# Kernel tuning notes

Measured on AMD Instinct MI355X. Metric: run time of the kernel, lower is better.

Reference implementation:

```python
import jax, jax.numpy as jnp
import numpy as np

TAU = 2.0        # LIF membrane time constant
ALPHA = 4.0      # spikingjelly default Sigmoid surrogate alpha
NUM_HEADS = 8

@jax.custom_vjp
def spike(x):
    return (x >= 0.0).astype(x.dtype)

def _spike_fwd(x):
    return spike(x), x

def _spike_bwd(x, g):
    s = jax.nn.sigmoid(ALPHA * x)
    return (g * ALPHA * s * (1.0 - s),)

spike.defvjp(_spike_fwd, _spike_bwd)

def lif(x_seq, v_th):
    """Multi-step LIF over leading time dim. Hard reset to 0, detach_reset."""
    def step(v, xt):
        h = v + (xt - v) / TAU
        s = spike(h - v_th)
        v_new = h * (1.0 - jax.lax.stop_gradient(s))
        return v_new, s
    _, s_seq = jax.lax.scan(step, jnp.zeros_like(x_seq[0]), x_seq)
    return s_seq

def bn_eval(x, w, b, m, v, eps=1e-5):
    # BatchNorm1d in eval mode over channel dim C (last axis here, since the
    # torch code transposes to (TB,C,N) purely to make C the channel axis).
    inv = w / jnp.sqrt(v + eps)
    return x * inv + (b - m * inv)

def setup_inputs() -> dict:
    key = jax.random.key(0)
    T, B, N, C = 4, 8, 512, 512
    ks = jax.random.split(key, 32)
    d = {"x": jax.random.normal(ks[0], (T, B, N, C), dtype=jnp.float32)}
    names = ["q", "k", "v", "p"]
    for i, nm in enumerate(names):
        kk = jax.random.split(ks[i + 1], 6)
        d[nm + "_w"] = jax.random.normal(kk[0], (C, C), dtype=jnp.float32) * (C ** -0.5)
        d[nm + "_b"] = jax.random.normal(kk[1], (C,), dtype=jnp.float32) * 0.01
        d[nm + "_bn_w"] = jax.random.uniform(kk[2], (C,), minval=0.5, maxval=1.5, dtype=jnp.float32)
        d[nm + "_bn_b"] = jax.random.normal(kk[3], (C,), dtype=jnp.float32) * 0.1
        d[nm + "_bn_m"] = jax.random.normal(kk[4], (C,), dtype=jnp.float32) * 0.1
        d[nm + "_bn_v"] = jax.random.uniform(kk[5], (C,), minval=0.5, maxval=1.5, dtype=jnp.float32)
    return d

def _forward(x, q_w, q_b, q_bn_w, q_bn_b, q_bn_m, q_bn_v,
             k_w, k_b, k_bn_w, k_bn_b, k_bn_m, k_bn_v,
             v_w, v_b, v_bn_w, v_bn_b, v_bn_m, v_bn_v,
             p_w, p_b, p_bn_w, p_bn_b, p_bn_m, p_bn_v):
    T, B, N, C = x.shape
    H = NUM_HEADS
    hd = C // H
    scale = hd ** -0.5

    def branch(w, b, bw, bb, bm, bv):
        y = jnp.einsum("tbnc,dc->tbnd", x, w) + b            # Linear
        y = bn_eval(y, bw, bb, bm, bv)                        # BN1d (eval)
        y = lif(y, 1.0)                                       # (T,B,N,C) spikes
        return y.reshape(T, B, N, H, hd).transpose(0, 1, 3, 2, 4)  # (T,B,H,N,hd)

    q = branch(q_w, q_b, q_bn_w, q_bn_b, q_bn_m, q_bn_v)
    k = branch(k_w, k_b, k_bn_w, k_bn_b, k_bn_m, k_bn_v)
    v = branch(v_w, v_b, v_bn_w, v_bn_b, v_bn_m, v_bn_v)

    gamma = 1.0 - 2.0 ** (-5.0 - jnp.arange(H, dtype=jnp.float32))
    idx = jnp.arange(N)
    dist = jnp.abs(idx[:, None] - idx[None, :]).astype(jnp.float32)  # bidirectional
    D = gamma[:, None, None] ** dist                                  # (H,N,N)

    attn = jnp.einsum("tbhnd,tbhmd->tbhnm", q, k) * scale * D
    out = jnp.einsum("tbhnm,tbhmd->tbhnd", attn, v)
    out = out.transpose(0, 1, 3, 2, 4).reshape(T, B, N, C)
    out = lif(out, 0.5)                                      # retention_lif, v_th=0.5

    y = jnp.einsum("tbnc,dc->tbnd", out, p_w) + p_b
    y = bn_eval(y, p_bn_w, p_bn_b, p_bn_m, p_bn_v)
    return lif(y, 1.0)

def reference(x, q_w, q_b, q_bn_w, q_bn_b, q_bn_m, q_bn_v,
              k_w, k_b, k_bn_w, k_bn_b, k_bn_m, k_bn_v,
              v_w, v_b, v_bn_w, v_bn_b, v_bn_m, v_bn_v,
              p_w, p_b, p_bn_w, p_bn_b, p_bn_m, p_bn_v):
    return _forward(x, q_w, q_b, q_bn_w, q_bn_b, q_bn_m, q_bn_v,
                    k_w, k_b, k_bn_w, k_bn_b, k_bn_m, k_bn_v,
                    v_w, v_b, v_bn_w, v_bn_b, v_bn_m, v_bn_v,
                    p_w, p_b, p_bn_w, p_bn_b, p_bn_m, p_bn_v)
```

## Files before the change

kernel.cpp:

```cpp
#include <hip/hip_runtime.h>
#include <cstdint>

typedef unsigned long long u64;

#define TPB 256
#define MARGIN 5e-4
#define FCAP (1 << 20)

typedef __bf16 bf16x8 __attribute__((ext_vector_type(8)));
typedef __bf16 bf16x4 __attribute__((ext_vector_type(4)));
typedef float f32x4 __attribute__((ext_vector_type(4)));

__global__ void init_kernel(double* __restrict__ pw, int* __restrict__ ctr) {
    int h = threadIdx.x;
    if (h < 8) {
        double gamma = 1.0 - ldexp(1.0, -5 - h);
        double p = 1.0;
        for (int i = 0; i < 512; ++i) { pw[h * 512 + i] = p; p *= gamma; }
        ctr[h] = 0;
    }
}

__global__ void split_all(const float* __restrict__ x,
                          const float* __restrict__ w0, const float* __restrict__ w1,
                          const float* __restrict__ w2, const float* __restrict__ w3,
                          __bf16* __restrict__ Xh, __bf16* __restrict__ Xl,
                          __bf16* __restrict__ Wsp) {
    int blk = blockIdx.x;
    const float* src; __bf16 *hi, *lo; size_t off;
    if (blk < 8192) {
        src = x; hi = Xh; lo = Xl; off = (size_t)blk * 1024;
    } else {
        int wb = blk - 8192;
        int br = wb >> 8;
        const float* ws[4] = {w0, w1, w2, w3};
        src = ws[br];
        hi = Wsp + (size_t)br * 524288;
        lo = hi + 262144;
        off = (size_t)(wb & 255) * 1024;
    }
    size_t i = off + threadIdx.x * 4;
    float4 v = *(const float4*)(src + i);
    bf16x4 h4, l4;
    #pragma unroll
    for (int e = 0; e < 4; ++e) {
        float f = (&v.x)[e];
        __bf16 hh = (__bf16)f;
        h4[e] = hh;
        l4[e] = (__bf16)(f - (float)hh);
    }
    *(bf16x4*)(hi + i) = h4;
    *(bf16x4*)(lo + i) = l4;
}

__global__ __launch_bounds__(256) void gemm_bn_mfma2(
    const __bf16* __restrict__ Ahg, const __bf16* __restrict__ Alg,
    const __bf16* __restrict__ Whg, const __bf16* __restrict__ Wlg,
    const float* __restrict__ bias,
    const float* __restrict__ bnw, const float* __restrict__ bnb,
    const float* __restrict__ bnm, const float* __restrict__ bnv,
    float* __restrict__ out, int asplit)
{
    __shared__ __bf16 AhS[128][40];
    __shared__ __bf16 AlS[128][40];
    __shared__ __bf16 WhS[128][40];
    __shared__ __bf16 WlS[128][40];

    const int tid = threadIdx.x;
    const int m0 = blockIdx.x * 128;
    const int d0 = blockIdx.y * 128;
    const int wv = tid >> 6;
    const int wm = wv >> 1;
    const int wd = wv & 1;
    const int lane = tid & 63;
    const int fr = lane & 15;
    const int fg = lane >> 4;
// ... 1 lines not shown
    const int sseg = (tid & 1) * 16;

    f32x4 acc[4][4];
    #pragma unroll
    for (int i = 0; i < 4; ++i)
        #pragma unroll
        for (int j = 0; j < 4; ++j)
            acc[i][j] = (f32x4){0.f, 0.f, 0.f, 0.f};

    for (int k0 = 0; k0 < 512; k0 += 32) {
        __syncthreads();
        {
            const __bf16* pa = Ahg + (size_t)(m0 + srow) * 512 + k0 + sseg;
            *(bf16x8*)&AhS[srow][sseg]     = *(const bf16x8*)pa;
            *(bf16x8*)&AhS[srow][sseg + 8] = *(const bf16x8*)(pa + 8);
            if (asplit) {
                const __bf16* pl = Alg + (size_t)(m0 + srow) * 512 + k0 + sseg;
                *(bf16x8*)&AlS[srow][sseg]     = *(const bf16x8*)pl;
                *(bf16x8*)&AlS[srow][sseg + 8] = *(const bf16x8*)(pl + 8);
            }
            const __bf16* pwh = Whg + (size_t)(d0 + srow) * 512 + k0 + sseg;
            const __bf16* pwl = Wlg + (size_t)(d0 + srow) * 512 + k0 + sseg;
            *(bf16x8*)&WhS[srow][sseg]     = *(const bf16x8*)pwh;
            *(bf16x8*)&WhS[srow][sseg + 8] = *(const bf16x8*)(pwh + 8);
            *(bf16x8*)&WlS[srow][sseg]     = *(const bf16x8*)pwl;
            *(bf16x8*)&WlS[srow][sseg + 8] = *(const bf16x8*)(pwl + 8);
        }
        __syncthreads();

        bf16x8 ah[4], bh[4], bl[4];
        #pragma unroll
        for (int i = 0; i < 4; ++i)
            ah[i] = *(const bf16x8*)&AhS[wm * 64 + i * 16 + fr][fg * 8];
        #pragma unroll
        for (int j = 0; j < 4; ++j) {
            bh[j] = *(const bf16x8*)&WhS[wd * 64 + j * 16 + fr][fg * 8];
            bl[j] = *(const bf16x8*)&WlS[wd * 64 + j * 16 + fr][fg * 8];
        }
        #pragma unroll
        for (int i = 0; i < 4; ++i)
            #pragma unroll
            for (int j = 0; j < 4; ++j) {
                acc[i][j] = __builtin_amdgcn_mfma_f32_16x16x32_bf16(ah[i], bh[j], acc[i][j], 0, 0, 0);
                acc[i][j] = __builtin_amdgcn_mfma_f32_16x16x32_bf16(ah[i], bl[j], acc[i][j], 0, 0, 0);
            }
        if (asplit) {
            bf16x8 al[4];
            #pragma unroll
            for (int i = 0; i < 4; ++i)
                al[i] = *(const bf16x8*)&AlS[wm * 64 + i * 16 + fr][fg * 8];
            #pragma unroll
            for (int i = 0; i < 4; ++i)
                #pragma unroll
                for (int j = 0; j < 4; ++j)
                    acc[i][j] = __builtin_amdgcn_mfma_f32_16x16x32_bf16(al[i], bh[j], acc[i][j], 0, 0, 0);
        }
    }

    #pragma unroll
    for (int j = 0; j < 4; ++j) {
        int d = d0 + wd * 64 + j * 16 + fr;
        double inv = (double)bnw[d] / sqrt((double)bnv[d] + 1e-5);
        double sh  = (double)bnb[d] - (double)bnm[d] * inv;
        double bs  = (double)bias[d];
        #pragma unroll
        for (int i = 0; i < 4; ++i) {
            #pragma unroll
            for (int reg = 0; reg < 4; ++reg) {
                int m = m0 + wm * 64 + i * 16 + fg * 4 + reg;
                out[(size_t)m * 512 + d] = (float)(((double)acc[i][j][reg] + bs) * inv + sh);
            }
        }
    }
}

__global__ __launch_bounds__(256) void gemm_bn_mfma(
    const float* __restrict__ A, const float* __restrict__ W,
    const float* __restrict__ bias,
    const float* __restrict__ bnw, const float* __restrict__ bnb,
    const float* __restrict__ bnm, const float* __restrict__ bnv,
    float* __restrict__ out)
{
    __shared__ __bf16 Ah[128][36];
    __shared__ __bf16 Al[128][36];
    __shared__ __bf16 Wh[64][36];
    __shared__ __bf16 Wl[64][36];

    const int tid = threadIdx.x;
    const int m0 = blockIdx.x * 128;
    const int d0 = blockIdx.y * 64;
    const int wv = tid >> 6;
    const int wm = wv >> 1;
    const int wd = wv & 1;
    const int lane = tid & 63;
    const int fr = lane & 15;
    const int fg = lane >> 4;
    const int srow = tid >> 3;
    const int scol = (tid & 7) * 4;

    f32x4 acc[4][2];
    #pragma unroll
    for (int i = 0; i < 4; ++i)
        #pragma unroll
        for (int j = 0; j < 2; ++j)
            acc[i][j] = (f32x4){0.f, 0.f, 0.f, 0.f};

    for (int k0 = 0; k0 < 512; k0 += 32) {
        __syncthreads();
        #pragma unroll
        for (int rep = 0; rep < 4; ++rep) {
            int row = srow + 32 * rep;
            float4 va = *(const float4*)(A + (size_t)(m0 + row) * 512 + k0 + scol);
            #pragma unroll
            for (int e = 0; e < 4; ++e) {
                float f = (&va.x)[e];
                __bf16 h = (__bf16)f;
                Ah[row][scol + e] = h;
                Al[row][scol + e] = (__bf16)(f - (float)h);
            }
        }
        #pragma unroll
        for (int rep = 0; rep < 2; ++rep) {
            int row = srow + 32 * rep;
            float4 vw = *(const float4*)(W + (size_t)(d0 + row) * 512 + k0 + scol);
            #pragma unroll
            for (int e = 0; e < 4; ++e) {
                float f = (&vw.x)[e];
                __bf16 h = (__bf16)f;
                Wh[row][scol + e] = h;
                Wl[row][scol + e] = (__bf16)(f - (float)h);
            }
        }
        __syncthreads();

        union FU { bf16x8 v8; struct { __bf16 a[4], b[4]; } s; };
        bf16x8 ah[4], al[4], bh[2], bl[2];
        #pragma unroll
        for (int i = 0; i < 4; ++i) {
            int row = wm * 64 + i * 16 + fr;
            FU u1, u2;
            *(double*)&u1.s.a[0] = *(const double*)&Ah[row][fg * 8];
            *(double*)&u1.s.b[0] = *(const double*)&Ah[row][fg * 8 + 4];
            *(double*)&u2.s.a[0] = *(const double*)&Al[row][fg * 8];
            *(double*)&u2.s.b[0] = *(const double*)&Al[row][fg * 8 + 4];
            ah[i] = u1.v8; al[i] = u2.v8;
        }
        #pragma unroll
        for (int j = 0; j < 2; ++j) {
            int row = wd * 32 + j * 16 + fr;
            FU u1, u2;
            *(double*)&u1.s.a[0] = *(const double*)&Wh[row][fg * 8];
            *(double*)&u1.s.b[0] = *(const double*)&Wh[row][fg * 8 + 4];
            *(double*)&u2.s.a[0] = *(const double*)&Wl[row][fg * 8];
            *(double*)&u2.s.b[0] = *(const double*)&Wl[row][fg * 8 + 4];
            bh[j] = u1.v8; bl[j] = u2.v8;
        }
        #pragma unroll
        for (int i = 0; i < 4; ++i)
            #pragma unroll
            for (int j = 0; j < 2; ++j) {
                acc[i][j] = __builtin_amdgcn_mfma_f32_16x16x32_bf16(ah[i], bh[j], acc[i][j], 0, 0, 0);
                acc[i][j] = __builtin_amdgcn_mfma_f32_16x16x32_bf16(ah[i], bl[j], acc[i][j], 0, 0, 0);
                acc[i][j] = __builtin_amdgcn_mfma_f32_16x16x32_bf16(al[i], bh[j], acc[i][j], 0, 0, 0);
            }
    }

    #pragma unroll
    for (int j = 0; j < 2; ++j) {
        int d = d0 + wd * 32 + j * 16 + fr;
        double inv = (double)bnw[d] / sqrt((double)bnv[d] + 1e-5);
        double sh  = (double)bnb[d] - (double)bnm[d] * inv;
        double bs  = (double)bias[d];
        #pragma unroll
        for (int i = 0; i < 4; ++i) {
            #pragma unroll
            for (int reg = 0; reg < 4; ++reg) {
                int m = m0 + wm * 64 + i * 16 + fg * 4 + reg;
                out[(size_t)m * 512 + d] = (float)(((double)acc[i][j][reg] + bs) * inv + sh);
            }
        }
    }
}

__global__ void lif_mask_flag(const float* __restrict__ Y, u64* __restrict__ msk,
                              int* __restrict__ ctr, int* __restrict__ list, int slot) {
    int g = blockIdx.x * TPB + threadIdx.x;
    int c = g & 511, n = (g >> 9) & 511, b = g >> 18;
    int h = c >> 6;
    int lane = threadIdx.x & 63;
    double v = 0.0;
    bool flag = false;
    for (int t = 0; t < 4; ++t) {
        float y = Y[((size_t)((t * 8 + b) * 512 + n) << 9) + c];
        double hh = v + ((double)y - v) * 0.5;
        flag |= fabs(hh - 1.0) < MARGIN;
        bool s = hh >= 1.0;
        u64 mk = __ballot(s);
        if (lane == 0) msk[((t * 8 + b) * 8 + h) * 512 + n] = mk;
        v = s ? 0.0 : hh;
    }
    if (flag) {
        int idx = atomicAdd(ctr + slot, 1);
        if (idx < FCAP) list[idx] = g;
    }
}

__global__ void fix_mask(const float* __restrict__ x, const float* __restrict__ w,
                         const float* __restrict__ bias,
                         const float* __restrict__ bnw, const float* __restrict__ bnb,
                         const float* __restrict__ bnm, const float* __restrict__ bnv,
                         u64* __restrict__ msk, const int* __restrict__ ctr,
                         const int* __restrict__ list, int slot) {
    int cnt = ctr[slot]; if (cnt > FCAP) cnt = FCAP;
    int wv = (blockIdx.x * blockDim.x + threadIdx.x) >> 6;
    int nw = (gridDim.x * blockDim.x) >> 6;
    int lane = threadIdx.x & 63;
    for (int i = wv; i < cnt; i += nw) {
        int g = list[i];
// ... 152 lines not shown
            }
        }
    }

    #pragma unroll
    for (int j2 = 0; j2 < 4; ++j2) {
        int c = h * 64 + j2 * 16 + fr;
        #pragma unroll
        for (int reg = 0; reg < 4; ++reg) {
            int n = n0 + wn + fg * 4 + reg;
            O[((size_t)(tb * 512 + n) << 9) + c] = acc_o[j2][reg];
        }
    }
}

__global__ void lif_ret_bf(const float* __restrict__ Y, __bf16* __restrict__ Rb,
                           int* __restrict__ ctr, int* __restrict__ list) {
    int g = blockIdx.x * TPB + threadIdx.x;
    int c = g & 511, n = (g >> 9) & 511, b = g >> 18;
    double v = 0.0, eb = 0.0;
    bool flag = false;
    for (int t = 0; t < 4; ++t) {
        size_t idx = ((size_t)((t * 8 + b) * 512 + n) << 9) + c;
        double x = (double)Y[idx];
        double hh = v + (x - v) * 0.5;
        eb = 0.5 * eb + 0.5 * (fabs(x) * 1e-4);
        flag |= fabs(hh - 0.5) <= eb + 1e-9;
        bool s = hh >= 0.5;
        Rb[idx] = s ? (__bf16)1.0f : (__bf16)0.0f;
        v = s ? 0.0 : hh;
        if (s) eb = 0.0;
    }
    if (flag) {
        int i2 = atomicAdd(ctr + 4, 1);
        if (i2 < FCAP) list[i2] = g;
    }
}

__global__ void lif_ret_f(const float* __restrict__ Y, float* __restrict__ R,
                          int* __restrict__ ctr, int* __restrict__ list) {
    int g = blockIdx.x * TPB + threadIdx.x;
    int c = g & 511, n = (g >> 9) & 511, b = g >> 18;
    double v = 0.0, eb = 0.0;
    bool flag = false;
    for (int t = 0; t < 4; ++t) {
        size_t idx = ((size_t)((t * 8 + b) * 512 + n) << 9) + c;
        double x = (double)Y[idx];
        double hh = v + (x - v) * 0.5;
        eb = 0.5 * eb + 0.5 * (fabs(x) * 1e-4);
        flag |= fabs(hh - 0.5) <= eb + 1e-9;
        bool s = hh >= 0.5;
        R[idx] = s ? 1.0f : 0.0f;
        v = s ? 0.0 : hh;
        if (s) eb = 0.0;
    }
    if (flag) {
        int i2 = atomicAdd(ctr + 4, 1);
        if (i2 < FCAP) list[i2] = g;
    }
}

__global__ void repair_ret_bf(const u64* __restrict__ qm, const u64* __restrict__ km,
                              const u64* __restrict__ vm, const double* __restrict__ pw,
                              const int* __restrict__ ctr, const int* __restrict__ list,
                              __bf16* __restrict__ Rb) {
    int cnt = ctr[4]; if (cnt > FCAP) cnt = FCAP;
    int wv = (blockIdx.x * blockDim.x + threadIdx.x) >> 6;
    int nw = (gridDim.x * blockDim.x) >> 6;
    int lane = threadIdx.x & 63;
    for (int i = wv; i < cnt; i += nw) {
        int g = list[i];
        int c = g & 511, n = (g >> 9) & 511, b = g >> 18;
        int h = c >> 6, d = c & 63;
        double acc_t[4];
        for (int t = 0; t < 4; ++t) {
            int base = ((t * 8 + b) * 8 + h) * 512;
            u64 qw = qm[base + n];
            double p = 0.0;
            for (int j = 0; j < 8; ++j) {
                int m = j * 64 + lane;
// ... 1 lines not shown
                u64 vvm = vm[base + m];
                if ((vvm >> d) & 1ull) {
                    int dist = n - m; if (dist < 0) dist = -dist;
                    p += (double)__popcll(qw & kk) * pw[h * 512 + dist];
                }
            }
            acc_t[t] = p;
        }
        #pragma unroll
        for (int off = 32; off; off >>= 1) {
            #pragma unroll
            for (int t = 0; t < 4; ++t) acc_t[t] += __shfl_xor(acc_t[t], off, 64);
        }
        if (lane == 0) {
            double v = 0.0;
            for (int t = 0; t < 4; ++t) {
                double x = acc_t[t] * 0.125;
                double hh = v + (x - v) * 0.5;
                bool s = hh >= 0.5;
                Rb[((size_t)((t * 8 + b) * 512 + n) << 9) + c] = s ? (__bf16)1.0f : (__bf16)0.0f;
                v = s ? 0.0 : hh;
            }
        }
    }
}

__global__ void repair_ret_f(const u64* __restrict__ qm, const u64* __restrict__ km,
                             const u64* __restrict__ vm, const double* __restrict__ pw,
                             const int* __restrict__ ctr, const int* __restrict__ list,
                             float* __restrict__ r) {
    int cnt = ctr[4]; if (cnt > FCAP) cnt = FCAP;
    int wv = (blockIdx.x * blockDim.x + threadIdx.x) >> 6;
    int nw = (gridDim.x * blockDim.x) >> 6;
    int lane = threadIdx.x & 63;
    for (int i = wv; i < cnt; i += nw) {
        int g = list[i];
        int c = g & 511, n = (g >> 9) & 511, b = g >> 18;
        int h = c >> 6, d = c & 63;
// ... 19 lines not shown
            for (int t = 0; t < 4; ++t) acc_t[t] += __shfl_xor(acc_t[t], off, 64);
        }
        if (lane == 0) {
            double v = 0.0;
            for (int t = 0; t < 4; ++t) {
                double x = acc_t[t] * 0.125;
                double hh = v + (x - v) * 0.5;
                bool s = hh >= 0.5;
                r[((size_t)((t * 8 + b) * 512 + n) << 9) + c] = s ? 1.0f : 0.0f;
                v = s ? 0.0 : hh;
            }
        }
    }
}

__global__ void final_lif_flag(float* __restrict__ Y, int* __restrict__ ctr,
                               int* __restrict__ list) {
    int g = blockIdx.x * TPB + threadIdx.x;
    int c = g & 511, n = (g >> 9) & 511, b = g >> 18;
    double v = 0.0;
    bool flag = false;
    for (int t = 0; t < 4; ++t) {
        size_t idx = ((size_t)((t * 8 + b) * 512 + n) << 9) + c;
        float y = Y[idx];
        double hh = v + ((double)y - v) * 0.5;
        flag |= fabs(hh - 1.0) < MARGIN;
        bool s = hh >= 1.0;
        Y[idx] = s ? 1.0f : 0.0f;
        v = s ? 0.0 : hh;
    }
    if (flag) {
        int idx = atomicAdd(ctr + 3, 1);
        if (idx < FCAP) list[idx] = g;
    }
}

__global__ void final_flag(const float* __restrict__ Y, int* __restrict__ ctr,
                           int* __restrict__ list) {
    int g = blockIdx.x * TPB + threadIdx.x;
    int c = g & 511, n = (g >> 9) & 511, b = g >> 18;
    double v = 0.0;
    bool flag = false;
    for (int t = 0; t < 4; ++t) {
        float y = Y[((size_t)((t * 8 + b) * 512 + n) << 9) + c];
        double hh = v + ((double)y - v) * 0.5;
        flag |= fabs(hh - 1.0) < MARGIN;
        bool s = hh >= 1.0;
        v = s ? 0.0 : hh;
    }
    if (flag) {
        int idx = atomicAdd(ctr + 3, 1);
        if (idx < FCAP) list[idx] = g;
    }
}

__global__ void final_write(const float* __restrict__ Y, float* __restrict__ out) {
    int g = blockIdx.x * TPB + threadIdx.x;
    int c = g & 511, n = (g >> 9) & 511, b = g >> 18;
    double v = 0.0;
    for (int t = 0; t < 4; ++t) {
        size_t idx = ((size_t)((t * 8 + b) * 512 + n) << 9) + c;
        float y = Y[idx];
        double hh = v + ((double)y - v) * 0.5;
        bool s = hh >= 1.0;
        out[idx] = s ? 1.0f : 0.0f;
        v = s ? 0.0 : hh;
    }
}

__global__ void fix_final_bf(const __bf16* __restrict__ rr, const float* __restrict__ w,
                             const float* __restrict__ bias,
                             const float* __restrict__ bnw, const float* __restrict__ bnb,
                             const float* __restrict__ bnm, const float* __restrict__ bnv,
                             const int* __restrict__ ctr, int* __restrict__ list) {
    int cnt = ctr[3]; if (cnt > FCAP) cnt = FCAP;
    int wv = (blockIdx.x * blockDim.x + threadIdx.x) >> 6;
    int nw = (gridDim.x * blockDim.x) >> 6;
    int lane = threadIdx.x & 63;
    for (int i = wv; i < cnt; i += nw) {
        int g = list[i] & 0x00FFFFFF;
        int c = g & 511, n = (g >> 9) & 511, b = g >> 18;
        const float* wr = w + (size_t)c * 512;
        double dot[4];
        #pragma unroll
        for (int t = 0; t < 4; ++t) {
            const __bf16* xr = rr + ((size_t)((t * 8 + b) * 512 + n) << 9);
            double p = 0.0;
            #pragma unroll
            for (int j = 0; j < 8; ++j)
                p += (double)(float)xr[lane + 64 * j] * (double)wr[lane + 64 * j];
            dot[t] = p;
        }
        #pragma unroll
        for (int off = 32; off; off >>= 1) {
            #pragma unroll
            for (int t = 0; t < 4; ++t)
                dot[t] += __shfl_xor(dot[t], off, 64);
        }
        if (lane == 0) {
            double inv = (double)bnw[c] / sqrt((double)bnv[c] + 1e-5);
            double sh  = (double)bnb[c] - (double)bnm[c] * inv;
            double bs  = (double)bias[c];
            double v = 0.0;
            int sp = 0;
            for (int t = 0; t < 4; ++t) {
                double y = (dot[t] + bs) * inv + sh;
                double hh = v + (y - v) * 0.5;
                bool s = hh >= 1.0;
                sp |= (s ? 1 : 0) << t;
                v = s ? 0.0 : hh;
            }
            list[i] = g | (sp << 24);
        }
    }
}

__global__ void fix_final_f(const float* __restrict__ rr, const float* __restrict__ w,
                            const float* __restrict__ bias,
                            const float* __restrict__ bnw, const float* __restrict__ bnb,
                            const float* __restrict__ bnm, const float* __restrict__ bnv,
                            const int* __restrict__ ctr, int* __restrict__ list) {
    int cnt = ctr[3]; if (cnt > FCAP) cnt = FCAP;
    int wv = (blockIdx.x * blockDim.x + threadIdx.x) >> 6;
    int nw = (gridDim.x * blockDim.x) >> 6;
    int lane = threadIdx.x & 63;
    for (int i = wv; i < cnt; i += nw) {
        int g = list[i] & 0x00FFFFFF;
        int c = g & 511, n = (g >> 9) & 511, b = g >> 18;
// ... 20 lines not shown
            double bs  = (double)bias[c];
            double v = 0.0;
            int sp = 0;
            for (int t = 0; t < 4; ++t) {
                double y = (dot[t] + bs) * inv + sh;
                double hh = v + (y - v) * 0.5;
                bool s = hh >= 1.0;
                sp |= (s ? 1 : 0) << t;
                v = s ? 0.0 : hh;
            }
            list[i] = g | (sp << 24);
        }
    }
}

__global__ void fix_scatter(const int* __restrict__ ctr, const int* __restrict__ list,
                            float* __restrict__ out) {
    int cnt = ctr[3]; if (cnt > FCAP) cnt = FCAP;
    int i = blockIdx.x * blockDim.x + threadIdx.x;
    if (i >= cnt) return;
    int e = list[i];
    int g = e & 0x00FFFFFF, sp = (e >> 24) & 0xF;
    int c = g & 511, n = (g >> 9) & 511, b = g >> 18;
    for (int t = 0; t < 4; ++t)
        out[((size_t)((t * 8 + b) * 512 + n) << 9) + c] = ((sp >> t) & 1) ? 1.0f : 0.0f;
}

extern "C" void kernel_launch(void* const* d_in, const int* in_sizes, int n_in,
                              void* d_out, int out_size, void* d_ws, size_t ws_size,
                              hipStream_t stream) {
// ... 21 lines not shown
    __bf16* Xh = (__bf16*)p;  p += NX * 2;
    __bf16* Xl = (__bf16*)p;  p += NX * 2;
    __bf16* Wsp = (__bf16*)p; p += (size_t)4 * 2 * 262144 * 2;
    size_t need_fast = (size_t)(p - (char*)d_ws);
    int fast = ws_size >= need_fast;

    init_kernel<<<1, 64, 0, stream>>>(pw, ctr);

    dim3 g2(128, 4);
    dim3 gg(128, 8);

    if (fast) {
        split_all<<<8192 + 1024, 256, 0, stream>>>(x, w[0], w[1], w[2], w[3], Xh, Xl, Wsp);
        for (int br = 0; br < 3; ++br) {
            u64* msk = br == 0 ? qm : (br == 1 ? km : vm);
            gemm_bn_mfma2<<<g2, 256, 0, stream>>>(Xh, Xl,
                Wsp + (size_t)br * 524288, Wsp + (size_t)br * 524288 + 262144,
                bi[br], bnw[br], bnb[br], bnm[br], bnv[br], Y, 1);
            lif_mask_flag<<<8192, TPB, 0, stream>>>(Y, msk, ctr, list, br);
            fix_mask<<<128, 256, 0, stream>>>(x, w[br], bi[br], bnw[br], bnb[br],
                                              bnm[br], bnv[br], msk, ctr, list, br);
        }
        ret_fused2<<<2048, 256, 0, stream>>>(qm, km, vm, pw, Y);
        lif_ret_bf<<<8192, TPB, 0, stream>>>(Y, Xh, ctr, list);
        repair_ret_bf<<<256, 256, 0, stream>>>(qm, km, vm, pw, ctr, list, Xh);
        gemm_bn_mfma2<<<g2, 256, 0, stream>>>(Xh, Xh,
            Wsp + (size_t)3 * 524288, Wsp + (size_t)3 * 524288 + 262144,
            bi[3], bnw[3], bnb[3], bnm[3], bnv[3], (float*)d_out, 0);
        final_lif_flag<<<8192, TPB, 0, stream>>>((float*)d_out, ctr, list);
        fix_final_bf<<<128, 256, 0, stream>>>(Xh, w[3], bi[3], bnw[3], bnb[3],
                                              bnm[3], bnv[3], ctr, list);
        fix_scatter<<<4096, 256, 0, stream>>>(ctr, list, (float*)d_out);
    } else {
        for (int br = 0; br < 3; ++br) {
            u64* msk = br == 0 ? qm : (br == 1 ? km : vm);
            gemm_bn_mfma<<<gg, 256, 0, stream>>>(x, w[br], bi[br], bnw[br], bnb[br],
                                                 bnm[br], bnv[br], Y);
            lif_mask_flag<<<8192, TPB, 0, stream>>>(Y, msk, ctr, list, br);
            fix_mask<<<128, 256, 0, stream>>>(x, w[br], bi[br], bnw[br], bnb[br],
                                              bnm[br], bnv[br], msk, ctr, list, br);
        }
        float* r = (float*)d_out;
        ret_fused2<<<2048, 256, 0, stream>>>(qm, km, vm, pw, Y);
        lif_ret_f<<<8192, TPB, 0, stream>>>(Y, r, ctr, list);
        repair_ret_f<<<256, 256, 0, stream>>>(qm, km, vm, pw, ctr, list, r);
        gemm_bn_mfma<<<gg, 256, 0, stream>>>(r, w[3], bi[3], bnw[3], bnb[3],
                                             bnm[3], bnv[3], Y);
// ... 8 lines not shown
```

Baseline: 326.9 us.

## Fuse LIF spike masking into GEMM epilogues and permute token layout

The bf16-split X is stored permuted so each GEMM tile row block holds all four timesteps of a token. That lets the LIF recurrence run inside the GEMM epilogue, writing bitmasks directly and removing the fp32 Y round trip and the separate lif_mask_flag kernel. The final projection GEMM likewise applies LIF and writes spikes straight to the output, with a direct fix kernel replacing the flag, fix and scatter passes. The retention LIF writes into the permuted layout, and the epilogue now does heavier double-precision work and scattered stores.

```diff
diff --git a/kernel.cpp b/kernel.cpp
--- a/kernel.cpp
+++ b/kernel.cpp
@@ -27,39 +27,51 @@
                           __bf16* __restrict__ Xh, __bf16* __restrict__ Xl,
                           __bf16* __restrict__ Wsp) {
     int blk = blockIdx.x;
-    const float* src; __bf16 *hi, *lo; size_t off;
     if (blk < 8192) {
-        src = x; hi = Xh; lo = Xl; off = (size_t)blk * 1024;
+        size_t i = (size_t)blk * 1024 + threadIdx.x * 4;
+        int m = (int)(i >> 9), c = (int)(i & 511);
+        int mp = (m & 4095) * 4 + (m >> 12);
+        float4 v = *(const float4*)(x + i);
+        bf16x4 h4, l4;
+        #pragma unroll
+        for (int e = 0; e < 4; ++e) {
+            float f = (&v.x)[e];
+            __bf16 hh = (__bf16)f;
+            h4[e] = hh;
+            l4[e] = (__bf16)(f - (float)hh);
+        }
+        size_t dst = (size_t)mp * 512 + c;
+        *(bf16x4*)(Xh + dst) = h4;
+        *(bf16x4*)(Xl + dst) = l4;
     } else {
         int wb = blk - 8192;
         int br = wb >> 8;
         const float* ws[4] = {w0, w1, w2, w3};
-        src = ws[br];
-        hi = Wsp + (size_t)br * 524288;
-        lo = hi + 262144;
-        off = (size_t)(wb & 255) * 1024;
-    }
-    size_t i = off + threadIdx.x * 4;
-    float4 v = *(const float4*)(src + i);
-    bf16x4 h4, l4;
-    #pragma unroll
-    for (int e = 0; e < 4; ++e) {
-        float f = (&v.x)[e];
-        __bf16 hh = (__bf16)f;
-        h4[e] = hh;
-        l4[e] = (__bf16)(f - (float)hh);
-    }
-    *(bf16x4*)(hi + i) = h4;
-    *(bf16x4*)(lo + i) = l4;
-}
-
-__global__ __launch_bounds__(256) void gemm_bn_mfma2(
+        const float* src = ws[br];
+        __bf16* hi = Wsp + (size_t)br * 524288;
+        __bf16* lo = hi + 262144;
+        size_t i = (size_t)(wb & 255) * 1024 + threadIdx.x * 4;
+        float4 v = *(const float4*)(src + i);
+        bf16x4 h4, l4;
+        #pragma unroll
+        for (int e = 0; e < 4; ++e) {
+            float f = (&v.x)[e];
+            __bf16 hh = (__bf16)f;
+            h4[e] = hh;
+            l4[e] = (__bf16)(f - (float)hh);
+        }
+        *(bf16x4*)(hi + i) = h4;
+        *(bf16x4*)(lo + i) = l4;
+    }
+}
+
+__global__ __launch_bounds__(256) void gemm_lif_mask(
     const __bf16* __restrict__ Ahg, const __bf16* __restrict__ Alg,
     const __bf16* __restrict__ Whg, const __bf16* __restrict__ Wlg,
     const float* __restrict__ bias,
     const float* __restrict__ bnw, const float* __restrict__ bnb,
     const float* __restrict__ bnm, const float* __restrict__ bnv,
-    float* __restrict__ out, int asplit)
+    u64* __restrict__ msk, int* __restrict__ ctr, int* __restrict__ list, int slot)
 {
     __shared__ __bf16 AhS[128][40];
     __shared__ __bf16 AlS[128][40];
@@ -91,11 +103,9 @@
             const __bf16* pa = Ahg + (size_t)(m0 + srow) * 512 + k0 + sseg;
             *(bf16x8*)&AhS[srow][sseg]     = *(const bf16x8*)pa;
             *(bf16x8*)&AhS[srow][sseg + 8] = *(const bf16x8*)(pa + 8);
-            if (asplit) {
-                const __bf16* pl = Alg + (size_t)(m0 + srow) * 512 + k0 + sseg;
-                *(bf16x8*)&AlS[srow][sseg]     = *(const bf16x8*)pl;
-                *(bf16x8*)&AlS[srow][sseg + 8] = *(const bf16x8*)(pl + 8);
-            }
+            const __bf16* pl = Alg + (size_t)(m0 + srow) * 512 + k0 + sseg;
+            *(bf16x8*)&AlS[srow][sseg]     = *(const bf16x8*)pl;
+            *(bf16x8*)&AlS[srow][sseg + 8] = *(const bf16x8*)(pl + 8);
             const __bf16* pwh = Whg + (size_t)(d0 + srow) * 512 + k0 + sseg;
             const __bf16* pwl = Wlg + (size_t)(d0 + srow) * 512 + k0 + sseg;
             *(bf16x8*)&WhS[srow][sseg]     = *(const bf16x8*)pwh;
@@ -121,164 +131,158 @@
                 acc[i][j] = __builtin_amdgcn_mfma_f32_16x16x32_bf16(ah[i], bh[j], acc[i][j], 0, 0, 0);
                 acc[i][j] = __builtin_amdgcn_mfma_f32_16x16x32_bf16(ah[i], bl[j], acc[i][j], 0, 0, 0);
             }
-        if (asplit) {
-            bf16x8 al[4];
-            #pragma unroll
-            for (int i = 0; i < 4; ++i)
-                al[i] = *(const bf16x8*)&AlS[wm * 64 + i * 16 + fr][fg * 8];
-            #pragma unroll
-            for (int i = 0; i < 4; ++i)
-                #pragma unroll
-                for (int j = 0; j < 4; ++j)
-                    acc[i][j] = __builtin_amdgcn_mfma_f32_16x16x32_bf16(al[i], bh[j], acc[i][j], 0, 0, 0);
-        }
-    }
-
+        bf16x8 al[4];
+        #pragma unroll
+        for (int i = 0; i < 4; ++i)
+            al[i] = *(const bf16x8*)&AlS[wm * 64 + i * 16 + fr][fg * 8];
+        #pragma unroll
+        for (int i = 0; i < 4; ++i)
+            #pragma unroll
+            for (int j = 0; j < 4; ++j)
+                acc[i][j] = __builtin_amdgcn_mfma_f32_16x16x32_bf16(al[i], bh[j], acc[i][j], 0, 0, 0);
+    }
+
+    double invj[4], shj[4], bsj[4];
     #pragma unroll
     for (int j = 0; j < 4; ++j) {
         int d = d0 + wd * 64 + j * 16 + fr;
-        double inv = (double)bnw[d] / sqrt((double)bnv[d] + 1e-5);
-        double sh  = (double)bnb[d] - (double)bnm[d] * inv;
-        double bs  = (double)bias[d];
-        #pragma unroll
-        for (int i = 0; i < 4; ++i) {
-            #pragma unroll
-            for (int reg = 0; reg < 4; ++reg) {
-                int m = m0 + wm * 64 + i * 16 + fg * 4 + reg;
-                out[(size_t)m * 512 + d] = (float)(((double)acc[i][j][reg] + bs) * inv + sh);
-            }
-        }
-    }
-}
-
-__global__ __launch_bounds__(256) void gemm_bn_mfma(
-    const float* __restrict__ A, const float* __restrict__ W,
+        invj[j] = (double)bnw[d] / sqrt((double)bnv[d] + 1e-5);
+        shj[j]  = (double)bnb[d] - (double)bnm[d] * invj[j];
+        bsj[j]  = (double)bias[d];
+    }
+    int hword = (d0 >> 6) + wd;
+    int bn0 = blockIdx.x * 32 + wm * 16;
+
+    #pragma unroll
+    for (int i = 0; i < 4; ++i) {
+        int bn = bn0 + i * 4 + fg;
+        int b = bn >> 9, n = bn & 511;
+        u64 w[4] = {0ull, 0ull, 0ull, 0ull};
+        #pragma unroll
+        for (int j = 0; j < 4; ++j) {
+            double v = 0.0;
+            bool fl = false;
+            #pragma unroll
+            for (int t = 0; t < 4; ++t) {
+                double y = ((double)acc[i][j][t] + bsj[j]) * invj[j] + shj[j];
+                double hh = v + (y - v) * 0.5;
+                fl |= fabs(hh - 1.0) < MARGIN;
+                bool s = hh >= 1.0;
+                u64 blt = __ballot(s);
+                w[t] |= ((blt >> (fg * 16)) & 0xFFFFull) << (j * 16);
+                v = s ? 0.0 : hh;
+            }
+            if (fl) {
+                int d = d0 + wd * 64 + j * 16 + fr;
+                int idx = atomicAdd(ctr + slot, 1);
+                if (idx < FCAP) list[idx] = (b << 18) | (n << 9) | d;
+            }
+        }
+        if (fr == 0) {
+            #pragma unroll
+            for (int t = 0; t < 4; ++t)
+                msk[((t * 8 + b) * 8 + hword) * 512 + n] = w[t];
+        }
+    }
+}
+
+__global__ __launch_bounds__(256) void gemm_final_lif(
+    const __bf16* __restrict__ Ahg,
+    const __bf16* __restrict__ Whg, const __bf16* __restrict__ Wlg,
     const float* __restrict__ bias,
     const float* __restrict__ bnw, const float* __restrict__ bnb,
     const float* __restrict__ bnm, const float* __restrict__ bnv,
-    float* __restrict__ out)
+    float* __restrict__ out, int* __restrict__ ctr, int* __restrict__ list)
 {
-    __shared__ __bf16 Ah[128][36];
-    __shared__ __bf16 Al[128][36];
-    __shared__ __bf16 Wh[64][36];
-    __shared__ __bf16 Wl[64][36];
+    __shared__ __bf16 AhS[128][40];
+    __shared__ __bf16 WhS[128][40];
+    __shared__ __bf16 WlS[128][40];
 
     const int tid = threadIdx.x;
     const int m0 = blockIdx.x * 128;
-    const int d0 = blockIdx.y * 64;
+    const int d0 = blockIdx.y * 128;
     const int wv = tid >> 6;
     const int wm = wv >> 1;
     const int wd = wv & 1;
     const int lane = tid & 63;
     const int fr = lane & 15;
     const int fg = lane >> 4;
-    const int srow = tid >> 3;
-    const int scol = (tid & 7) * 4;
-
-    f32x4 acc[4][2];
+    const int srow = tid >> 1;
+    const int sseg = (tid & 1) * 16;
+
+    f32x4 acc[4][4];
     #pragma unroll
     for (int i = 0; i < 4; ++i)
         #pragma unroll
-        for (int j = 0; j < 2; ++j)
+        for (int j = 0; j < 4; ++j)
             acc[i][j] = (f32x4){0.f, 0.f, 0.f, 0.f};
 
     for (int k0 = 0; k0 < 512; k0 += 32) {
         __syncthreads();
-        #pragma unroll
-        for (int rep = 0; rep < 4; ++rep) {
-            int row = srow + 32 * rep;
-            float4 va = *(const float4*)(A + (size_t)(m0 + row) * 512 + k0 + scol);
-            #pragma unroll
-            for (int e = 0; e < 4; ++e) {
-                float f = (&va.x)[e];
-                __bf16 h = (__bf16)f;
-                Ah[row][scol + e] = h;
-                Al[row][scol + e] = (__bf16)(f - (float)h);
-            }
-        }
-        #pragma unroll
-        for (int rep = 0; rep < 2; ++rep) {
-            int row = srow + 32 * rep;
-            float4 vw = *(const float4*)(W + (size_t)(d0 + row) * 512 + k0 + scol);
-            #pragma unroll
-            for (int e = 0; e < 4; ++e) {
-                float f = (&vw.x)[e];
-                __bf16 h = (__bf16)f;
-                Wh[row][scol + e] = h;
-                Wl[row][scol + e] = (__bf16)(f - (float)h);
-            }
+        {
+            const __bf16* pa = Ahg + (size_t)(m0 + srow) * 512 + k0 + sseg;
+            *(bf16x8*)&AhS[srow][sseg]     = *(const bf16x8*)pa;
+            *(bf16x8*)&AhS[srow][sseg + 8] = *(const bf16x8*)(pa + 8);
+            const __bf16* pwh = Whg + (size_t)(d0 + srow) * 512 + k0 + sseg;
+            const __bf16* pwl = Wlg + (size_t)(d0 + srow) * 512 + k0 + sseg;
+            *(bf16x8*)&WhS[srow][sseg]     = *(const bf16x8*)pwh;
+            *(bf16x8*)&WhS[srow][sseg + 8] = *(const bf16x8*)(pwh + 8);
+            *(bf16x8*)&WlS[srow][sseg]     = *(const bf16x8*)pwl;
+            *(bf16x8*)&WlS[srow][sseg + 8] = *(const bf16x8*)(pwl + 8);
         }
         __syncthreads();
 
-        union FU { bf16x8 v8; struct { __bf16 a[4], b[4]; } s; };
-        bf16x8 ah[4], al[4], bh[2], bl[2];
-        #pragma unroll
-        for (int i = 0; i < 4; ++i) {
-            int row = wm * 64 + i * 16 + fr;
-            FU u1, u2;
-            *(double*)&u1.s.a[0] = *(const double*)&Ah[row][fg * 8];
-            *(double*)&u1.s.b[0] = *(const double*)&Ah[row][fg * 8 + 4];
-            *(double*)&u2.s.a[0] = *(const double*)&Al[row][fg * 8];
-            *(double*)&u2.s.b[0] = *(const double*)&Al[row][fg * 8 + 4];
-            ah[i] = u1.v8; al[i] = u2.v8;
-        }
-        #pragma unroll
-        for (int j = 0; j < 2; ++j) {
-            int row = wd * 32 + j * 16 + fr;
-            FU u1, u2;
-            *(double*)&u1.s.a[0] = *(const double*)&Wh[row][fg * 8];
-            *(double*)&u1.s.b[0] = *(const double*)&Wh[row][fg * 8 + 4];
-            *(double*)&u2.s.a[0] = *(const double*)&Wl[row][fg * 8];
-            *(double*)&u2.s.b[0] = *(const double*)&Wl[row][fg * 8 + 4];
-            bh[j] = u1.v8; bl[j] = u2.v8;
-        }
+        bf16x8 ah[4], bh[4], bl[4];
         #pragma unroll
         for (int i = 0; i < 4; ++i)
-            #pragma unroll
-            for (int j = 0; j < 2; ++j) {
+            ah[i] = *(const bf16x8*)&AhS[wm * 64 + i * 16 + fr][fg * 8];
+        #pragma unroll
+        for (int j = 0; j < 4; ++j) {
+            bh[j] = *(const bf16x8*)&WhS[wd * 64 + j * 16 + fr][fg * 8];
+            bl[j] = *(const bf16x8*)&WlS[wd * 64 + j * 16 + fr][fg * 8];
+        }
+        #pragma unroll
+        for (int i = 0; i < 4; ++i)
+            #pragma unroll
+            for (int j = 0; j < 4; ++j) {
                 acc[i][j] = __builtin_amdgcn_mfma_f32_16x16x32_bf16(ah[i], bh[j], acc[i][j], 0, 0, 0);
                 acc[i][j] = __builtin_amdgcn_mfma_f32_16x16x32_bf16(ah[i], bl[j], acc[i][j], 0, 0, 0);
-                acc[i][j] = __builtin_amdgcn_mfma_f32_16x16x32_bf16(al[i], bh[j], acc[i][j], 0, 0, 0);
-            }
-    }
-
-    #pragma unroll
-    for (int j = 0; j < 2; ++j) {
-        int d = d0 + wd * 32 + j * 16 + fr;
-        double inv = (double)bnw[d] / sqrt((double)bnv[d] + 1e-5);
-        double sh  = (double)bnb[d] - (double)bnm[d] * inv;
-        double bs  = (double)bias[d];
-        #pragma unroll
-        for (int i = 0; i < 4; ++i) {
-            #pragma unroll
-            for (int reg = 0; reg < 4; ++reg) {
-                int m = m0 + wm * 64 + i * 16 + fg * 4 + reg;
-                out[(size_t)m * 512 + d] = (float)(((double)acc[i][j][reg] + bs) * inv + sh);
-            }
-        }
-    }
-}
-
-__global__ void lif_mask_flag(const float* __restrict__ Y, u64* __restrict__ msk,
-                              int* __restrict__ ctr, int* __restrict__ list, int slot) {
-    int g = blockIdx.x * TPB + threadIdx.x;
-    int c = g & 511, n = (g >> 9) & 511, b = g >> 18;
-    int h = c >> 6;
-    int lane = threadIdx.x & 63;
-    double v = 0.0;
-    bool flag = false;
-    for (int t = 0; t < 4; ++t) {
-        float y = Y[((size_t)((t * 8 + b) * 512 + n) << 9) + c];
-        double hh = v + ((double)y - v) * 0.5;
-        flag |= fabs(hh - 1.0) < MARGIN;
-        bool s = hh >= 1.0;
-        u64 mk = __ballot(s);
-        if (lane == 0) msk[((t * 8 + b) * 8 + h) * 512 + n] = mk;
-        v = s ? 0.0 : hh;
-    }
-    if (flag) {
-        int idx = atomicAdd(ctr + slot, 1);
-        if (idx < FCAP) list[idx] = g;
+            }
+    }
+
+    double invj[4], shj[4], bsj[4];
+    #pragma unroll
+    for (int j = 0; j < 4; ++j) {
+        int d = d0 + wd * 64 + j * 16 + fr;
+        invj[j] = (double)bnw[d] / sqrt((double)bnv[d] + 1e-5);
+        shj[j]  = (double)bnb[d] - (double)bnm[d] * invj[j];
+        bsj[j]  = (double)bias[d];
+    }
+    int bn0 = blockIdx.x * 32 + wm * 16;
+
+    #pragma unroll
+    for (int i = 0; i < 4; ++i) {
+        int bn = bn0 + i * 4 + fg;
+        int b = bn >> 9, n = bn & 511;
+        #pragma unroll
+        for (int j = 0; j < 4; ++j) {
+            int d = d0 + wd * 64 + j * 16 + fr;
+            double v = 0.0;
+            bool fl = false;
+            #pragma unroll
+            for (int t = 0; t < 4; ++t) {
+                double y = ((double)acc[i][j][t] + bsj[j]) * invj[j] + shj[j];
+                double hh = v + (y - v) * 0.5;
+                fl |= fabs(hh - 1.0) < MARGIN;
+                bool s = hh >= 1.0;
+                out[((size_t)((t * 8 + b) * 512 + n) << 9) + d] = s ? 1.0f : 0.0f;
+                v = s ? 0.0 : hh;
+            }
+            if (fl) {
+                int idx = atomicAdd(ctr + 3, 1);
+                if (idx < FCAP) list[idx] = (b << 18) | (n << 9) | d;
+            }
+        }
     }
 }
 
@@ -461,10 +465,11 @@
     }
 }
 
-__global__ void lif_ret_bf(const float* __restrict__ Y, __bf16* __restrict__ Rb,
-                           int* __restrict__ ctr, int* __restrict__ list) {
+__global__ void lif_ret_bf2(const float* __restrict__ Y, __bf16* __restrict__ Rb,
+                            int* __restrict__ ctr, int* __restrict__ list) {
     int g = blockIdx.x * TPB + threadIdx.x;
     int c = g & 511, n = (g >> 9) & 511, b = g >> 18;
+    size_t pbase = ((size_t)(b * 512 + n) * 4) * 512 + c;
     double v = 0.0, eb = 0.0;
     bool flag = false;
     for (int t = 0; t < 4; ++t) {
@@ -474,7 +479,7 @@
         eb = 0.5 * eb + 0.5 * (fabs(x) * 1e-4);
         flag |= fabs(hh - 0.5) <= eb + 1e-9;
         bool s = hh >= 0.5;
-        Rb[idx] = s ? (__bf16)1.0f : (__bf16)0.0f;
+        Rb[pbase + (size_t)t * 512] = s ? (__bf16)1.0f : (__bf16)0.0f;
         v = s ? 0.0 : hh;
         if (s) eb = 0.0;
     }
@@ -484,33 +489,10 @@
     }
 }
 
-__global__ void lif_ret_f(const float* __restrict__ Y, float* __restrict__ R,
-                          int* __restrict__ ctr, int* __restrict__ list) {
-    int g = blockIdx.x * TPB + threadIdx.x;
-    int c = g & 511, n = (g >> 9) & 511, b = g >> 18;
-    double v = 0.0, eb = 0.0;
-    bool flag = false;
-    for (int t = 0; t < 4; ++t) {
-        size_t idx = ((size_t)((t * 8 + b) * 512 + n) << 9) + c;
-        double x = (double)Y[idx];
-        double hh = v + (x - v) * 0.5;
-        eb = 0.5 * eb + 0.5 * (fabs(x) * 1e-4);
-        flag |= fabs(hh - 0.5) <= eb + 1e-9;
-        bool s = hh >= 0.5;
-        R[idx] = s ? 1.0f : 0.0f;
-        v = s ? 0.0 : hh;
-        if (s) eb = 0.0;
-    }
-    if (flag) {
-        int i2 = atomicAdd(ctr + 4, 1);
-        if (i2 < FCAP) list[i2] = g;
-    }
-}
-
-__global__ void repair_ret_bf(const u64* __restrict__ qm, const u64* __restrict__ km,
-                              const u64* __restrict__ vm, const double* __restrict__ pw,
-                              const int* __restrict__ ctr, const int* __restrict__ list,
-                              __bf16* __restrict__ Rb) {
+__global__ void repair_ret_bf2(const u64* __restrict__ qm, const u64* __restrict__ km,
+                               const u64* __restrict__ vm, const double* __restrict__ pw,
+                               const int* __restrict__ ctr, const int* __restrict__ list,
+                               __bf16* __restrict__ Rb) {
     int cnt = ctr[4]; if (cnt > FCAP) cnt = FCAP;
     int wv = (blockIdx.x * blockDim.x + threadIdx.x) >> 6;
     int nw = (gridDim.x * blockDim.x) >> 6;
@@ -542,14 +524,215 @@
         }
         if (lane == 0) {
             double v = 0.0;
+            size_t pbase = ((size_t)(b * 512 + n) * 4) * 512 + c;
             for (int t = 0; t < 4; ++t) {
                 double x = acc_t[t] * 0.125;
                 double hh = v + (x - v) * 0.5;
                 bool s = hh >= 0.5;
-                Rb[((size_t)((t * 8 + b) * 512 + n) << 9) + c] = s ? (__bf16)1.0f : (__bf16)0.0f;
+                Rb[pbase + (size_t)t * 512] = s ? (__bf16)1.0f : (__bf16)0.0f;
                 v = s ? 0.0 : hh;
             }
         }
+    }
+}
+
+__global__ void fix_final_direct(const __bf16* __restrict__ rr, const float* __restrict__ w,
+                                 const float* __restrict__ bias,
+                                 const float* __restrict__ bnw, const float* __restrict__ bnb,
+                                 const float* __restrict__ bnm, const float* __restrict__ bnv,
+                                 const int* __restrict__ ctr, const int* __restrict__ list,
+                                 float* __restrict__ out) {
+    int cnt = ctr[3]; if (cnt > FCAP) cnt = FCAP;
+    int wv = (blockIdx.x * blockDim.x + threadIdx.x) >> 6;
+    int nw = (gridDim.x * blockDim.x) >> 6;
+    int lane = threadIdx.x & 63;
+    for (int i = wv; i < cnt; i += nw) {
+        int g = list[i];
+        int c = g & 511, n = (g >> 9) & 511, b = g >> 18;
+        const float* wr = w + (size_t)c * 512;
+        double dot[4];
+        #pragma unroll
+        for (int t = 0; t < 4; ++t) {
+            const __bf16* xr = rr + ((size_t)(b * 512 + n) * 4 + t) * 512;
+            double p = 0.0;
+            #pragma unroll
+            for (int j = 0; j < 8; ++j)
+                p += (double)(float)xr[lane + 64 * j] * (double)wr[lane + 64 * j];
+            dot[t] = p;
+        }
+        #pragma unroll
+        for (int off = 32; off; off >>= 1) {
+            #pragma unroll
+            for (int t = 0; t < 4; ++t)
+                dot[t] += __shfl_xor(dot[t], off, 64);
+        }
+        if (lane == 0) {
+            double inv = (double)bnw[c] / sqrt((double)bnv[c] + 1e-5);
+            double sh  = (double)bnb[c] - (double)bnm[c] * inv;
+            double bs  = (double)bias[c];
+            double v = 0.0;
+            for (int t = 0; t < 4; ++t) {
+                double y = (dot[t] + bs) * inv + sh;
+                double hh = v + (y - v) * 0.5;
+                bool s = hh >= 1.0;
+                out[((size_t)((t * 8 + b) * 512 + n) << 9) + c] = s ? 1.0f : 0.0f;
+                v = s ? 0.0 : hh;
+            }
+        }
+    }
+}
+
+__global__ __launch_bounds__(256) void gemm_bn_mfma(
+    const float* __restrict__ A, const float* __restrict__ W,
+    const float* __restrict__ bias,
+    const float* __restrict__ bnw, const float* __restrict__ bnb,
+    const float* __restrict__ bnm, const float* __restrict__ bnv,
+    float* __restrict__ out)
+{
+    __shared__ __bf16 Ah[128][36];
+    __shared__ __bf16 Al[128][36];
+    __shared__ __bf16 Wh[64][36];
+    __shared__ __bf16 Wl[64][36];
+
+    const int tid = threadIdx.x;
+    const int m0 = blockIdx.x * 128;
+    const int d0 = blockIdx.y * 64;
+    const int wv = tid >> 6;
+    const int wm = wv >> 1;
+    const int wd = wv & 1;
+    const int lane = tid & 63;
+    const int fr = lane & 15;
+    const int fg = lane >> 4;
+    const int srow = tid >> 3;
+    const int scol = (tid & 7) * 4;
+
+    f32x4 acc[4][2];
+    #pragma unroll
+    for (int i = 0; i < 4; ++i)
+        #pragma unroll
+        for (int j = 0; j < 2; ++j)
+            acc[i][j] = (f32x4){0.f, 0.f, 0.f, 0.f};
+
+    for (int k0 = 0; k0 < 512; k0 += 32) {
+        __syncthreads();
+        #pragma unroll
+        for (int rep = 0; rep < 4; ++rep) {
+            int row = srow + 32 * rep;
+            float4 va = *(const float4*)(A + (size_t)(m0 + row) * 512 + k0 + scol);
+            #pragma unroll
+            for (int e = 0; e < 4; ++e) {
+                float f = (&va.x)[e];
+                __bf16 h = (__bf16)f;
+                Ah[row][scol + e] = h;
+                Al[row][scol + e] = (__bf16)(f - (float)h);
+            }
+        }
+        #pragma unroll
+        for (int rep = 0; rep < 2; ++rep) {
+            int row = srow + 32 * rep;
+            float4 vw = *(const float4*)(W + (size_t)(d0 + row) * 512 + k0 + scol);
+            #pragma unroll
+            for (int e = 0; e < 4; ++e) {
+                float f = (&vw.x)[e];
+                __bf16 h = (__bf16)f;
+                Wh[row][scol + e] = h;
+                Wl[row][scol + e] = (__bf16)(f - (float)h);
+            }
+        }
+        __syncthreads();
+
+        union FU { bf16x8 v8; struct { __bf16 a[4], b[4]; } s; };
+        bf16x8 ah[4], al[4], bh[2], bl[2];
+        #pragma unroll
+        for (int i = 0; i < 4; ++i) {
+            int row = wm * 64 + i * 16 + fr;
+            FU u1, u2;
+            *(double*)&u1.s.a[0] = *(const double*)&Ah[row][fg * 8];
+            *(double*)&u1.s.b[0] = *(const double*)&Ah[row][fg * 8 + 4];
+            *(double*)&u2.s.a[0] = *(const double*)&Al[row][fg * 8];
+            *(double*)&u2.s.b[0] = *(const double*)&Al[row][fg * 8 + 4];
+            ah[i] = u1.v8; al[i] = u2.v8;
+        }
+        #pragma unroll
+        for (int j = 0; j < 2; ++j) {
+            int row = wd * 32 + j * 16 + fr;
+            FU u1, u2;
+            *(double*)&u1.s.a[0] = *(const double*)&Wh[row][fg * 8];
+            *(double*)&u1.s.b[0] = *(const double*)&Wh[row][fg * 8 + 4];
+            *(double*)&u2.s.a[0] = *(const double*)&Wl[row][fg * 8];
+            *(double*)&u2.s.b[0] = *(const double*)&Wl[row][fg * 8 + 4];
+            bh[j] = u1.v8; bl[j] = u2.v8;
+        }
+        #pragma unroll
+        for (int i = 0; i < 4; ++i)
+            #pragma unroll
+            for (int j = 0; j < 2; ++j) {
+                acc[i][j] = __builtin_amdgcn_mfma_f32_16x16x32_bf16(ah[i], bh[j], acc[i][j], 0, 0, 0);
+                acc[i][j] = __builtin_amdgcn_mfma_f32_16x16x32_bf16(ah[i], bl[j], acc[i][j], 0, 0, 0);
+                acc[i][j] = __builtin_amdgcn_mfma_f32_16x16x32_bf16(al[i], bh[j], acc[i][j], 0, 0, 0);
+            }
+    }
+
+    #pragma unroll
+    for (int j = 0; j < 2; ++j) {
+        int d = d0 + wd * 32 + j * 16 + fr;
+        double inv = (double)bnw[d] / sqrt((double)bnv[d] + 1e-5);
+        double sh  = (double)bnb[d] - (double)bnm[d] * inv;
+        double bs  = (double)bias[d];
+        #pragma unroll
+        for (int i = 0; i < 4; ++i) {
+            #pragma unroll
+            for (int reg = 0; reg < 4; ++reg) {
+                int m = m0 + wm * 64 + i * 16 + fg * 4 + reg;
+                out[(size_t)m * 512 + d] = (float)(((double)acc[i][j][reg] + bs) * inv + sh);
+            }
+        }
+    }
+}
+
+__global__ void lif_mask_flag(const float* __restrict__ Y, u64* __restrict__ msk,
+                              int* __restrict__ ctr, int* __restrict__ list, int slot) {
+    int g = blockIdx.x * TPB + threadIdx.x;
+    int c = g & 511, n = (g >> 9) & 511, b = g >> 18;
+    int h = c >> 6;
+    int lane = threadIdx.x & 63;
+    double v = 0.0;
+    bool flag = false;
+    for (int t = 0; t < 4; ++t) {
+        float y = Y[((size_t)((t * 8 + b) * 512 + n) << 9) + c];
+        double hh = v + ((double)y - v) * 0.5;
+        flag |= fabs(hh - 1.0) < MARGIN;
+        bool s = hh >= 1.0;
+        u64 mk = __ballot(s);
+        if (lane == 0) msk[((t * 8 + b) * 8 + h) * 512 + n] = mk;
+        v = s ? 0.0 : hh;
+    }
+    if (flag) {
+        int idx = atomicAdd(ctr + slot, 1);
+        if (idx < FCAP) list[idx] = g;
+    }
+}
+
+__global__ void lif_ret_f(const float* __restrict__ Y, float* __restrict__ R,
+                          int* __restrict__ ctr, int* __restrict__ list) {
+    int g = blockIdx.x * TPB + threadIdx.x;
+    int c = g & 511, n = (g >> 9) & 511, b = g >> 18;
+    double v = 0.0, eb = 0.0;
+    bool flag = false;
+    for (int t = 0; t < 4; ++t) {
+        size_t idx = ((size_t)((t * 8 + b) * 512 + n) << 9) + c;
+        double x = (double)Y[idx];
+        double hh = v + (x - v) * 0.5;
+        eb = 0.5 * eb + 0.5 * (fabs(x) * 1e-4);
+        flag |= fabs(hh - 0.5) <= eb + 1e-9;
+        bool s = hh >= 0.5;
+        R[idx] = s ? 1.0f : 0.0f;
+        v = s ? 0.0 : hh;
+        if (s) eb = 0.0;
+    }
+    if (flag) {
+        int i2 = atomicAdd(ctr + 4, 1);
+        if (i2 < FCAP) list[i2] = g;
     }
 }
 
@@ -599,27 +782,6 @@
     }
 }
 
-__global__ void final_lif_flag(float* __restrict__ Y, int* __restrict__ ctr,
-                               int* __restrict__ list) {
-    int g = blockIdx.x * TPB + threadIdx.x;
-    int c = g & 511, n = (g >> 9) & 511, b = g >> 18;
-    double v = 0.0;
-    bool flag = false;
-    for (int t = 0; t < 4; ++t) {
-        size_t idx = ((size_t)((t * 8 + b) * 512 + n) << 9) + c;
-        float y = Y[idx];
-        double hh = v + ((double)y - v) * 0.5;
-        flag |= fabs(hh - 1.0) < MARGIN;
-        bool s = hh >= 1.0;
-        Y[idx] = s ? 1.0f : 0.0f;
-        v = s ? 0.0 : hh;
-    }
-    if (flag) {
-        int idx = atomicAdd(ctr + 3, 1);
-        if (idx < FCAP) list[idx] = g;
-    }
-}
-
 __global__ void final_flag(const float* __restrict__ Y, int* __restrict__ ctr,
                            int* __restrict__ list) {
     int g = blockIdx.x * TPB + threadIdx.x;
@@ -636,67 +798,6 @@
     if (flag) {
         int idx = atomicAdd(ctr + 3, 1);
         if (idx < FCAP) list[idx] = g;
-    }
-}
-
-__global__ void final_write(const float* __restrict__ Y, float* __restrict__ out) {
-    int g = blockIdx.x * TPB + threadIdx.x;
-    int c = g & 511, n = (g >> 9) & 511, b = g >> 18;
-    double v = 0.0;
-    for (int t = 0; t < 4; ++t) {
-        size_t idx = ((size_t)((t * 8 + b) * 512 + n) << 9) + c;
-        float y = Y[idx];
-        double hh = v + ((double)y - v) * 0.5;
-        bool s = hh >= 1.0;
-        out[idx] = s ? 1.0f : 0.0f;
-        v = s ? 0.0 : hh;
-    }
-}
-
-__global__ void fix_final_bf(const __bf16* __restrict__ rr, const float* __restrict__ w,
-                             const float* __restrict__ bias,
-                             const float* __restrict__ bnw, const float* __restrict__ bnb,
-                             const float* __restrict__ bnm, const float* __restrict__ bnv,
-                             const int* __restrict__ ctr, int* __restrict__ list) {
-    int cnt = ctr[3]; if (cnt > FCAP) cnt = FCAP;
-    int wv = (blockIdx.x * blockDim.x + threadIdx.x) >> 6;
-    int nw = (gridDim.x * blockDim.x) >> 6;
-    int lane = threadIdx.x & 63;
-    for (int i = wv; i < cnt; i += nw) {
-        int g = list[i] & 0x00FFFFFF;
-        int c = g & 511, n = (g >> 9) & 511, b = g >> 18;
-        const float* wr = w + (size_t)c * 512;
-        double dot[4];
-        #pragma unroll
-        for (int t = 0; t < 4; ++t) {
-            const __bf16* xr = rr + ((size_t)((t * 8 + b) * 512 + n) << 9);
-            double p = 0.0;
-            #pragma unroll
-            for (int j = 0; j < 8; ++j)
-                p += (double)(float)xr[lane + 64 * j] * (double)wr[lane + 64 * j];
-            dot[t] = p;
-        }
-        #pragma unroll
-        for (int off = 32; off; off >>= 1) {
-            #pragma unroll
-            for (int t = 0; t < 4; ++t)
-                dot[t] += __shfl_xor(dot[t], off, 64);
-        }
-        if (lane == 0) {
-            double inv = (double)bnw[c] / sqrt((double)bnv[c] + 1e-5);
-            double sh  = (double)bnb[c] - (double)bnm[c] * inv;
-            double bs  = (double)bias[c];
-            double v = 0.0;
-            int sp = 0;
-            for (int t = 0; t < 4; ++t) {
-                double y = (dot[t] + bs) * inv + sh;
-                double hh = v + (y - v) * 0.5;
-                bool s = hh >= 1.0;
-                sp |= (s ? 1 : 0) << t;
-                v = s ? 0.0 : hh;
-            }
-            list[i] = g | (sp << 24);
-        }
     }
 }
 
@@ -747,6 +848,20 @@
     }
 }
 
+__global__ void final_write(const float* __restrict__ Y, float* __restrict__ out) {
+    int g = blockIdx.x * TPB + threadIdx.x;
+    int c = g & 511, n = (g >> 9) & 511, b = g >> 18;
+    double v = 0.0;
+    for (int t = 0; t < 4; ++t) {
+        size_t idx = ((size_t)((t * 8 + b) * 512 + n) << 9) + c;
+        float y = Y[idx];
+        double hh = v + ((double)y - v) * 0.5;
+        bool s = hh >= 1.0;
+        out[idx] = s ? 1.0f : 0.0f;
+        v = s ? 0.0 : hh;
+    }
+}
+
 __global__ void fix_scatter(const int* __restrict__ ctr, const int* __restrict__ list,
                             float* __restrict__ out) {
     int cnt = ctr[3]; if (cnt > FCAP) cnt = FCAP;
@@ -798,23 +913,20 @@
         split_all<<<8192 + 1024, 256, 0, stream>>>(x, w[0], w[1], w[2], w[3], Xh, Xl, Wsp);
         for (int br = 0; br < 3; ++br) {
             u64* msk = br == 0 ? qm : (br == 1 ? km : vm);
-            gemm_bn_mfma2<<<g2, 256, 0, stream>>>(Xh, Xl,
+            gemm_lif_mask<<<g2, 256, 0, stream>>>(Xh, Xl,
                 Wsp + (size_t)br * 524288, Wsp + (size_t)br * 524288 + 262144,
-                bi[br], bnw[br], bnb[br], bnm[br], bnv[br], Y, 1);
-            lif_mask_flag<<<8192, TPB, 0, stream>>>(Y, msk, ctr, list, br);
+                bi[br], bnw[br], bnb[br], bnm[br], bnv[br], msk, ctr, list, br);
             fix_mask<<<128, 256, 0, stream>>>(x, w[br], bi[br], bnw[br], bnb[br],
                                               bnm[br], bnv[br], msk, ctr, list, br);
         }
         ret_fused2<<<2048, 256, 0, stream>>>(qm, km, vm, pw, Y);
-        lif_ret_bf<<<8192, TPB, 0, stream>>>(Y, Xh, ctr, list);
-        repair_ret_bf<<<256, 256, 0, stream>>>(qm, km, vm, pw, ctr, list, Xh);
-        gemm_bn_mfma2<<<g2, 256, 0, stream>>>(Xh, Xh,
+        lif_ret_bf2<<<8192, TPB, 0, stream>>>(Y, Xh, ctr, list);
+        repair_ret_bf2<<<256, 256, 0, stream>>>(qm, km, vm, pw, ctr, list, Xh);
+        gemm_final_lif<<<g2, 256, 0, stream>>>(Xh,
             Wsp + (size_t)3 * 524288, Wsp + (size_t)3 * 524288 + 262144,
-            bi[3], bnw[3], bnb[3], bnm[3], bnv[3], (float*)d_out, 0);
-        final_lif_flag<<<8192, TPB, 0, stream>>>((float*)d_out, ctr, list);
-        fix_final_bf<<<128, 256, 0, stream>>>(Xh, w[3], bi[3], bnw[3], bnb[3],
-                                              bnm[3], bnv[3], ctr, list);
-        fix_scatter<<<4096, 256, 0, stream>>>(ctr, list, (float*)d_out);
+            bi[3], bnw[3], bnb[3], bnm[3], bnv[3], (float*)d_out, ctr, list);
+        fix_final_direct<<<128, 256, 0, stream>>>(Xh, w[3], bi[3], bnw[3], bnb[3],
+                                                  bnm[3], bnv[3], ctr, list, (float*)d_out);
     } else {
         for (int br = 0; br < 3; ++br) {
             u64* msk = br == 0 ? qm : (br == 1 ? km : vm);
```

Result: faster. 282.5 us (-13.6%).
